# Kernel tuning notes

Measured on AMD Instinct MI355X. Metric: run time of the kernel, lower is better.

## Reference

```python
import jax, jax.numpy as jnp
import numpy as np

C = 64
K = 3  # kernel_size
B, H, W = 8, 128, 128


def conv2d(x, w, b, pad, groups=1):
    y = jax.lax.conv_general_dilated(
        x, w, window_strides=(1, 1), padding=[(pad, pad), (pad, pad)],
        feature_group_count=groups, dimension_numbers=('NCHW', 'OIHW', 'NCHW'))
    return y + b[None, :, None, None]


def setup_inputs() -> dict:
    key = jax.random.key(0)
    ks = jax.random.split(key, 11)
    s3 = 1.0 / np.sqrt(C * 9)  # kaiming-ish scale for 3x3 convs
    inp = {
        'x':  jax.random.normal(ks[0], (B, C, H, W), jnp.float32),
        'w0': jax.random.normal(ks[1], (C, C, 3, 3), jnp.float32) * s3,
        'b0': jax.random.normal(ks[2], (C,), jnp.float32) * 0.01,
        'w1': jax.random.normal(ks[3], (C, 1, 3, 3), jnp.float32) * (1.0 / 3.0),  # depthwise
        'b1': jax.random.normal(ks[4], (C,), jnp.float32) * 0.01,
        'w2': jax.random.normal(ks[5], (1, 1, K), jnp.float32) * (1.0 / np.sqrt(K)),  # conv1d over channel axis
        'b2': jax.random.normal(ks[6], (1,), jnp.float32) * 0.01,
        'w3': jax.random.normal(ks[7], (C * K * K, C, 1, 1), jnp.float32) * (1.0 / np.sqrt(C)),  # 1x1 -> dynamic filters
        'b3': jax.random.normal(ks[8], (C * K * K,), jnp.float32) * 0.01,
        'wf': jax.random.normal(ks[9], (C, C, 3, 3), jnp.float32) * s3,
        'bf': jax.random.normal(ks[10], (C,), jnp.float32) * 0.01,
    }
    return inp


def reference(x, w0, b0, w1, b1, w2, b2, w3, b3, wf, bf):
    b, c, h, w = x.shape
    pre = x
    # conv0: dense 3x3
    x0 = conv2d(x, w0, b0, pad=1)
    # conv1: depthwise 3x3
    x1 = conv2d(x0, w1, b1, pad=1, groups=c)
    # ECA-style channel attention: global avg pool -> conv1d over channel dim
    m = jnp.mean(x0, axis=(2, 3))  # [b, c]
    x2 = jax.lax.conv_general_dilated(
        m[:, None, :], w2, window_strides=(1,), padding=[(K // 2, K // 2)],
        dimension_numbers=('NCH', 'OIH', 'NCH')) + b2[None, :, None]  # [b, 1, c]
    out = x1 + x2[:, 0, :, None, None]  # broadcast [b,c,1,1] over h,w
    # conv3: 1x1 producing per-pixel dynamic filters [b, c*9, h, w]
    fil = jnp.einsum('oc,bchw->bohw', w3[:, :, 0, 0], out) + b3[None, :, None, None]
    filter_x = fil.reshape(b, c, K * K, h, w)
    # unfold(x0): 3x3 patches, channel-major then row-major kernel positions
    xp = jnp.pad(x0, ((0, 0), (0, 0), (1, 1), (1, 1)))
    unfold_x = jnp.stack(
        [xp[:, :, i:i + h, j:j + w] for i in range(3) for j in range(3)], axis=2)  # [b,c,9,h,w]
    out = jnp.sum(unfold_x * filter_x, axis=2)  # per-pixel dynamic conv
    out = jnp.where(out >= 0, out, 0.2 * out)  # LeakyReLU(0.2)
    out = conv2d(out, wf, bf, pad=1) + pre
    return out
```

## Files before the change

### kernel.cpp

```cpp
#include <hip/hip_runtime.h>

#define BB 8
#define C 64
#define HH 128
#define WW 128
#define HW (HH*WW)

#define TS 72
#define NPX 324

typedef __attribute__((ext_vector_type(8))) short short8;
typedef __attribute__((ext_vector_type(4))) short short4v;
typedef __attribute__((ext_vector_type(4))) float f32x4;

__device__ inline unsigned short f2bf(float f) {
    union { float f; unsigned u; } v; v.f = f;
    unsigned r = v.u + 0x7fff + ((v.u >> 16) & 1);
    return (unsigned short)(r >> 16);
}
__device__ inline float bf2f(unsigned short h) {
    union { unsigned u; float f; } v; v.u = ((unsigned)h) << 16;
    return v.f;
}

__global__ __launch_bounds__(256) void prep_kernel(
    const float* __restrict__ w0, const float* __restrict__ wf,
    const float* __restrict__ w3, const float* __restrict__ b3,
    unsigned short* __restrict__ wb0, unsigned short* __restrict__ wbf,
    unsigned short* __restrict__ wb3, float* __restrict__ b3r,
    float* __restrict__ m)
{
    const int t = blockIdx.x * 256 + threadIdx.x;
    for (int i = t; i < C*C*9; i += 32*256) {
        int p = i % 9; int rest = i / 9; int ci = rest % C; int oc = rest / C;
        wb0[(p*C + oc)*C + ci] = f2bf(w0[i]);
        wbf[(p*C + oc)*C + ci] = f2bf(wf[i]);
    }
    for (int i = t; i < 9*C*C; i += 32*256) {
        int j = i >> 12, oc = (i >> 6) & 63, k = i & 63;
        wb3[i] = f2bf(w3[(oc*9 + j)*C + k]);
    }
    for (int i = t; i < 9*C; i += 32*256) {
        int j = i >> 6, oc = i & 63;
        b3r[i] = b3[oc*9 + j];
    }
    for (int i = t; i < BB*C; i += 32*256) m[i] = 0.f;
}

__global__ __launch_bounds__(256) void conv0_kernel(
    const float* __restrict__ x,
    const unsigned short* __restrict__ wb,
    const float* __restrict__ bias,
    unsigned short* __restrict__ x0g)
{
    __shared__ unsigned short tile[NPX*TS];
    const int b  = blockIdx.z;
    const int h0 = blockIdx.y * 16;
    const int w0 = blockIdx.x * 16;
    const int t  = threadIdx.x;

    {
        const int pxi = t & 31, g = t >> 5;
        for (int px = pxi; px < NPX; px += 32) {
            int th = px / 18, tw = px - th*18;
            int gh = h0 + th - 1, gw = w0 + tw - 1;
            short8 v = {0,0,0,0,0,0,0,0};
            if ((unsigned)gh < HH && (unsigned)gw < WW) {
                const float* sp = x + ((size_t)(b*C + g*8)*HW + gh*WW + gw);
#pragma unroll
                for (int k = 0; k < 8; ++k) v[k] = (short)f2bf(sp[k*HW]);
            }
            *(short8*)&tile[px*TS + g*8] = v;
        }
    }
    __syncthreads();

    const int wid = t >> 6, ln = t & 63;
    const int l15 = ln & 15, q = ln >> 4;

    f32x4 acc[4][4];
#pragma unroll
    for (int nt = 0; nt < 4; ++nt)
#pragma unroll
        for (int mt = 0; mt < 4; ++mt) acc[nt][mt] = (f32x4){0.f,0.f,0.f,0.f};

#pragma unroll
    for (int p = 0; p < 9; ++p) {
        const int dh = p / 3, dw = p % 3;
#pragma unroll
        for (int ks = 0; ks < 2; ++ks) {
            short8 af[4];
#pragma unroll
            for (int mt = 0; mt < 4; ++mt)
                af[mt] = *(const short8*)&wb[((size_t)(p*C) + mt*16 + l15)*C + ks*32 + q*8];
            short8 bf[4];
#pragma unroll
            for (int nt = 0; nt < 4; ++nt)
                bf[nt] = *(const short8*)&tile[((wid*4+nt+dh)*18 + l15 + dw)*TS + ks*32 + q*8];
#pragma unroll
            for (int nt = 0; nt < 4; ++nt)
#pragma unroll
                for (int mt = 0; mt < 4; ++mt)
                    acc[nt][mt] = __builtin_amdgcn_mfma_f32_16x16x32_bf16(
                        af[mt], bf[nt], acc[nt][mt], 0, 0, 0);
        }
    }

#pragma unroll
    for (int nt = 0; nt < 4; ++nt) {
        const int hh = h0 + wid*4 + nt;
        const size_t base = ((size_t)(b*HW) + hh*WW + w0 + l15)*C;
#pragma unroll
        for (int mt = 0; mt < 4; ++mt) {
            const int oc0 = mt*16 + q*4;
            const float4 bv = *(const float4*)&bias[oc0];
            unsigned u0 = (unsigned)f2bf(acc[nt][mt][0] + bv.x)
                        | ((unsigned)f2bf(acc[nt][mt][1] + bv.y) << 16);
            unsigned u1 = (unsigned)f2bf(acc[nt][mt][2] + bv.z)
                        | ((unsigned)f2bf(acc[nt][mt][3] + bv.w) << 16);
            uint2 uu; uu.x = u0; uu.y = u1;
            *(uint2*)&x0g[base + oc0] = uu;
        }
    }
}

__global__ __launch_bounds__(256) void mean_kernel(
    const unsigned short* __restrict__ x0, float* __restrict__ m)
{
    const int b = blockIdx.x >> 4, slice = blockIdx.x & 15;
    const int t = threadIdx.x;
    const int pxi = t >> 3, g = t & 7;
    const unsigned short* base = x0 + ((size_t)b*HW + slice*1024)*C + g*8;
    float s[8];
#pragma unroll
    for (int k = 0; k < 8; ++k) s[k] = 0.f;
    for (int it = 0; it < 32; ++it) {
        short8 v = *(const short8*)&base[(size_t)(it*32 + pxi)*C];
#pragma unroll
        for (int k = 0; k < 8; ++k) s[k] += bf2f((unsigned short)v[k]);
    }
    __shared__ float red[32][64];
#pragma unroll
    for (int k = 0; k < 8; ++k) red[pxi][g*8+k] = s[k];
    __syncthreads();
    if (t < 64) {
        float acc = 0.f;
        for (int i = 0; i < 32; ++i) acc += red[i][t];
        atomicAdd(&m[b*C + t], acc * (1.f/(float)HW));
    }
}

__global__ __launch_bounds__(256, 4) void dw_eca_kernel(
    const unsigned short* __restrict__ x0,
    const float* __restrict__ w1, const float* __restrict__ b1,
    const float* __restrict__ w2, const float* __restrict__ b2,
    const float* __restrict__ m,
    unsigned short* __restrict__ aout)
{
    const int tg = blockIdx.x * 256 + threadIdx.x;
    const int b = tg >> 14, px = tg & 16383;
    const int h = px >> 7, w = px & 127;
    const unsigned short* xb = x0 + (size_t)(b*HW)*C;
    const float w2a = w2[0], w2b = w2[1], w2c = w2[2], b2v = b2[0];

#pragma unroll
    for (int g = 0; g < 8; ++g) {
        float dw8[8];
#pragma unroll
        for (int k = 0; k < 8; ++k) dw8[k] = 0.f;
#pragma unroll
        for (int j = 0; j < 9; ++j) {
            const int nh = h + j/3 - 1, nw = w + j%3 - 1;
            short8 v = {0,0,0,0,0,0,0,0};
            if ((unsigned)nh < HH && (unsigned)nw < WW)
                v = *(const short8*)&xb[(size_t)(nh*WW + nw)*C + g*8];
#pragma unroll
            for (int k = 0; k < 8; ++k)
                dw8[k] = fmaf(w1[(g*8+k)*9 + j], bf2f((unsigned short)v[k]), dw8[k]);
        }
        short8 o;
#pragma unroll
        for (int k = 0; k < 8; ++k) {
            const int c = g*8 + k;
            const float mc = m[b*C + c];
            const float mp = (c > 0)  ? m[b*C + c - 1] : 0.f;
            const float mn = (c < 63) ? m[b*C + c + 1] : 0.f;
            const float att = fmaf(w2a, mp, fmaf(w2b, mc, fmaf(w2c, mn, b2v)));
            o[k] = (short)f2bf(dw8[k] + b1[c] + att);
        }
        *(short8*)&aout[(size_t)(b*HW + px)*C + g*8] = o;
    }
}

__global__ __launch_bounds__(256) void dynconv_kernel(
    const unsigned short* __restrict__ x0,
    const unsigned short* __restrict__ aout,
    const unsigned short* __restrict__ wb3,
    const float* __restrict__ b3r,
    unsigned short* __restrict__ yg)
{
    __shared__ unsigned short tile[NPX*TS];
    const int b  = blockIdx.z;
    const int h0 = blockIdx.y * 16;
    const int w0 = blockIdx.x * 16;
    const int t  = threadIdx.x;

    {
        const int pxi = t & 31, g = t >> 5;
        for (int px = pxi; px < NPX; px += 32) {
            int th = px / 18, tw = px - th*18;
            int gh = h0 + th - 1, gw = w0 + tw - 1;
            short8 v = {0,0,0,0,0,0,0,0};
            if ((unsigned)gh < HH && (unsigned)gw < WW)
                v = *(const short8*)&x0[((size_t)(b*HW) + gh*WW + gw)*C + g*8];
            *(short8*)&tile[px*TS + g*8] = v;
        }
    }
    __syncthreads();

    const int wid = t >> 6, ln = t & 63;
    const int l15 = ln & 15, q = ln >> 4;
    const int rl0 = wid*4;

    short8 pfrag[4][2];
#pragma unroll
    for (int nt = 0; nt < 4; ++nt) {
        const size_t pbase = ((size_t)(b*HW) + (h0+rl0+nt)*WW + w0 + l15)*C;
#pragma unroll
        for (int ks = 0; ks < 2; ++ks)
            pfrag[nt][ks] = *(const short8*)&aout[pbase + ks*32 + q*8];
    }

#pragma unroll
    for (int og = 0; og < 4; ++og) {
        f32x4 yac[4];
#pragma unroll
        for (int nt = 0; nt < 4; ++nt) yac[nt] = (f32x4){0.f,0.f,0.f,0.f};

        for (int j = 0; j < 9; ++j) {
            const int dh = j / 3, dw = j - dh*3;
            const f32x4 seed = *(const f32x4*)&b3r[j*64 + og*16 + q*4];
            const size_t abase = ((size_t)(j*64 + og*16 + l15))*C;
            const short8 a0 = *(const short8*)&wb3[abase + q*8];
            const short8 a1 = *(const short8*)&wb3[abase + 32 + q*8];
#pragma unroll
            for (int nt = 0; nt < 4; ++nt) {
                f32x4 fil = __builtin_amdgcn_mfma_f32_16x16x32_bf16(
                    a0, pfrag[nt][0], seed, 0, 0, 0);
                fil = __builtin_amdgcn_mfma_f32_16x16x32_bf16(
                    a1, pfrag[nt][1], fil, 0, 0, 0);
                const short4v pv = *(const short4v*)
                    &tile[((rl0+nt+dh)*18 + l15 + dw)*TS + og*16 + q*4];
#pragma unroll
                for (int reg = 0; reg < 4; ++reg)
                    yac[nt][reg] = fmaf(fil[reg],
                        bf2f((unsigned short)pv[reg]), yac[nt][reg]);
            }
        }

#pragma unroll
        for (int nt = 0; nt < 4; ++nt) {
            const size_t base = ((size_t)(b*HW) + (h0+rl0+nt)*WW + w0 + l15)*C;
            f32x4 v = yac[nt];
#pragma unroll
            for (int reg = 0; reg < 4; ++reg)
                v[reg] = (v[reg] >= 0.f) ? v[reg] : 0.2f * v[reg];
            unsigned u0 = (unsigned)f2bf(v[0]) | ((unsigned)f2bf(v[1]) << 16);
            unsigned u1 = (unsigned)f2bf(v[2]) | ((unsigned)f2bf(v[3]) << 16);
            uint2 uu; uu.x = u0; uu.y = u1;
            *(uint2*)&yg[base + og*16 + q*4] = uu;
        }
    }
}

__global__ __launch_bounds__(256) void convf_kernel(
    const unsigned short* __restrict__ yg,
    const unsigned short* __restrict__ wb,
    const float* __restrict__ bias,
    const float* __restrict__ res,
    float* __restrict__ outg)
{
    __shared__ unsigned short tile[NPX*TS];
    const int b  = blockIdx.z;
    const int h0 = blockIdx.y * 16;
    const int w0 = blockIdx.x * 16;
    const int t  = threadIdx.x;

    {
        const int pxi = t & 31, g = t >> 5;
        for (int px = pxi; px < NPX; px += 32) {
            int th = px / 18, tw = px - th*18;
            int gh = h0 + th - 1, gw = w0 + tw - 1;
            short8 v = {0,0,0,0,0,0,0,0};
            if ((unsigned)gh < HH && (unsigned)gw < WW)
                v = *(const short8*)&yg[((size_t)(b*HW) + gh*WW + gw)*C + g*8];
            *(short8*)&tile[px*TS + g*8] = v;
        }
    }
    __syncthreads();

    const int wid = t >> 6, ln = t & 63;
    const int l15 = ln & 15, q = ln >> 4;

    f32x4 acc[4][4];
#pragma unroll
    for (int mg = 0; mg < 4; ++mg)
#pragma unroll
        for (int nt = 0; nt < 4; ++nt) acc[mg][nt] = (f32x4){0.f,0.f,0.f,0.f};

#pragma unroll
    for (int p = 0; p < 9; ++p) {
        const int dh = p / 3, dw = p % 3;
#pragma unroll
        for (int ks = 0; ks < 2; ++ks) {
            short8 bfrag[4];
#pragma unroll
            for (int nt = 0; nt < 4; ++nt)
                bfrag[nt] = *(const short8*)&wb[((size_t)(p*C) + nt*16 + l15)*C + ks*32 + q*8];
            short8 afrag[4];
#pragma unroll
            for (int mg = 0; mg < 4; ++mg)
                afrag[mg] = *(const short8*)&tile[((wid*4+mg+dh)*18 + l15 + dw)*TS + ks*32 + q*8];
#pragma unroll
            for (int mg = 0; mg < 4; ++mg)
#pragma unroll
                for (int nt = 0; nt < 4; ++nt)
                    acc[mg][nt] = __builtin_amdgcn_mfma_f32_16x16x32_bf16(
                        afrag[mg], bfrag[nt], acc[mg][nt], 0, 0, 0);
        }
    }

#pragma unroll
    for (int mg = 0; mg < 4; ++mg) {
        const int hh = h0 + wid*4 + mg;
#pragma unroll
        for (int nt = 0; nt < 4; ++nt) {
            const int oc = nt*16 + l15;
            const float bv = bias[oc];
            const size_t base = (size_t)(b*C + oc)*HW + hh*WW + w0 + q*4;
            const float4 rv = *(const float4*)&res[base];
            float4 ov;
            ov.x = acc[mg][nt][0] + bv + rv.x;
            ov.y = acc[mg][nt][1] + bv + rv.y;
            ov.z = acc[mg][nt][2] + bv + rv.z;
            ov.w = acc[mg][nt][3] + bv + rv.w;
            *(float4*)&outg[base] = ov;
        }
    }
}

extern "C" void kernel_launch(void* const* d_in, const int* in_sizes, int n_in,
                              void* d_out, int out_size, void* d_ws, size_t ws_size,
                              hipStream_t stream) {
    const float* x  = (const float*)d_in[0];
    const float* w0 = (const float*)d_in[1];
    const float* b0 = (const float*)d_in[2];
    const float* w1 = (const float*)d_in[3];
    const float* b1 = (const float*)d_in[4];
    const float* w2 = (const float*)d_in[5];
    const float* b2 = (const float*)d_in[6];
    const float* w3 = (const float*)d_in[7];
    const float* b3 = (const float*)d_in[8];
    const float* wf = (const float*)d_in[9];
    const float* bf = (const float*)d_in[10];
    float* out = (float*)d_out;

    unsigned short* x0  = (unsigned short*)d_ws;
    unsigned short* y   = x0  + (size_t)BB*HW*C;
    unsigned short* ao  = y   + (size_t)BB*HW*C;
    float*          m   = (float*)(ao + (size_t)BB*HW*C);
    unsigned short* wb0 = (unsigned short*)(m + BB*C);
    unsigned short* wbf = wb0 + 9*C*C;
    unsigned short* wb3 = wbf + 9*C*C;
    float*          b3r = (float*)(wb3 + 9*C*C);

    prep_kernel<<<32, 256, 0, stream>>>(w0, wf, w3, b3, wb0, wbf, wb3, b3r, m);
    conv0_kernel<<<dim3(8,8,8), 256, 0, stream>>>(x, wb0, b0, x0);
    mean_kernel<<<128, 256, 0, stream>>>(x0, m);
    dw_eca_kernel<<<512, 256, 0, stream>>>(x0, w1, b1, w2, b2, m, ao);
    dynconv_kernel<<<dim3(8,8,8), 256, 0, stream>>>(x0, ao, wb3, b3r, y);
    convf_kernel<<<dim3(8,8,8), 256, 0, stream>>>(y, wbf, bf, x, out);
}
```

Baseline: 252.7 us.

## Fuse depthwise+ECA into dynamic conv kernel and double block threads

The depthwise 3x3 conv plus ECA attention is now computed inside the dynamic-filter kernel from the already-loaded x0 halo tile. Its output is kept in a swizzled LDS buffer instead of a global intermediate, which removes one kernel launch and a full write and read of the activation tensor. conv0 and convf move to 512 threads per block, with each wave covering 2 rows instead of 4 and the output-channel groups split across waves in the fused kernel. The larger LDS footprint (about 80KB per block) and 512-thread blocks may lower occupancy.

```diff
diff --git a/kernel.cpp b/kernel.cpp
--- a/kernel.cpp
+++ b/kernel.cpp
@@ -47,7 +47,7 @@
     for (int i = t; i < BB*C; i += 32*256) m[i] = 0.f;
 }
 
-__global__ __launch_bounds__(256) void conv0_kernel(
+__global__ __launch_bounds__(512) void conv0_kernel(
     const float* __restrict__ x,
     const unsigned short* __restrict__ wb,
     const float* __restrict__ bias,
@@ -60,8 +60,8 @@
     const int t  = threadIdx.x;
 
     {
-        const int pxi = t & 31, g = t >> 5;
-        for (int px = pxi; px < NPX; px += 32) {
+        const int pxi = t & 63, g = t >> 6;
+        for (int px = pxi; px < NPX; px += 64) {
             int th = px / 18, tw = px - th*18;
             int gh = h0 + th - 1, gw = w0 + tw - 1;
             short8 v = {0,0,0,0,0,0,0,0};
@@ -78,9 +78,9 @@
     const int wid = t >> 6, ln = t & 63;
     const int l15 = ln & 15, q = ln >> 4;
 
-    f32x4 acc[4][4];
-#pragma unroll
-    for (int nt = 0; nt < 4; ++nt)
+    f32x4 acc[2][4];
+#pragma unroll
+    for (int nt = 0; nt < 2; ++nt)
 #pragma unroll
         for (int mt = 0; mt < 4; ++mt) acc[nt][mt] = (f32x4){0.f,0.f,0.f,0.f};
 
@@ -93,12 +93,12 @@
 #pragma unroll
             for (int mt = 0; mt < 4; ++mt)
                 af[mt] = *(const short8*)&wb[((size_t)(p*C) + mt*16 + l15)*C + ks*32 + q*8];
-            short8 bf[4];
-#pragma unroll
-            for (int nt = 0; nt < 4; ++nt)
-                bf[nt] = *(const short8*)&tile[((wid*4+nt+dh)*18 + l15 + dw)*TS + ks*32 + q*8];
-#pragma unroll
-            for (int nt = 0; nt < 4; ++nt)
+            short8 bf[2];
+#pragma unroll
+            for (int nt = 0; nt < 2; ++nt)
+                bf[nt] = *(const short8*)&tile[((wid*2+nt+dh)*18 + l15 + dw)*TS + ks*32 + q*8];
+#pragma unroll
+            for (int nt = 0; nt < 2; ++nt)
 #pragma unroll
                 for (int mt = 0; mt < 4; ++mt)
                     acc[nt][mt] = __builtin_amdgcn_mfma_f32_16x16x32_bf16(
@@ -107,8 +107,8 @@
     }
 
 #pragma unroll
-    for (int nt = 0; nt < 4; ++nt) {
-        const int hh = h0 + wid*4 + nt;
+    for (int nt = 0; nt < 2; ++nt) {
+        const int hh = h0 + wid*2 + nt;
         const size_t base = ((size_t)(b*HW) + hh*WW + w0 + l15)*C;
 #pragma unroll
         for (int mt = 0; mt < 4; ++mt) {
@@ -150,64 +150,25 @@
     }
 }
 
-__global__ __launch_bounds__(256, 4) void dw_eca_kernel(
+__global__ __launch_bounds__(512) void fused_dyn_kernel(
     const unsigned short* __restrict__ x0,
     const float* __restrict__ w1, const float* __restrict__ b1,
     const float* __restrict__ w2, const float* __restrict__ b2,
-    const float* __restrict__ m,
-    unsigned short* __restrict__ aout)
-{
-    const int tg = blockIdx.x * 256 + threadIdx.x;
-    const int b = tg >> 14, px = tg & 16383;
-    const int h = px >> 7, w = px & 127;
-    const unsigned short* xb = x0 + (size_t)(b*HW)*C;
-    const float w2a = w2[0], w2b = w2[1], w2c = w2[2], b2v = b2[0];
-
-#pragma unroll
-    for (int g = 0; g < 8; ++g) {
-        float dw8[8];
-#pragma unroll
-        for (int k = 0; k < 8; ++k) dw8[k] = 0.f;
-#pragma unroll
-        for (int j = 0; j < 9; ++j) {
-            const int nh = h + j/3 - 1, nw = w + j%3 - 1;
-            short8 v = {0,0,0,0,0,0,0,0};
-            if ((unsigned)nh < HH && (unsigned)nw < WW)
-                v = *(const short8*)&xb[(size_t)(nh*WW + nw)*C + g*8];
-#pragma unroll
-            for (int k = 0; k < 8; ++k)
-                dw8[k] = fmaf(w1[(g*8+k)*9 + j], bf2f((unsigned short)v[k]), dw8[k]);
-        }
-        short8 o;
-#pragma unroll
-        for (int k = 0; k < 8; ++k) {
-            const int c = g*8 + k;
-            const float mc = m[b*C + c];
-            const float mp = (c > 0)  ? m[b*C + c - 1] : 0.f;
-            const float mn = (c < 63) ? m[b*C + c + 1] : 0.f;
-            const float att = fmaf(w2a, mp, fmaf(w2b, mc, fmaf(w2c, mn, b2v)));
-            o[k] = (short)f2bf(dw8[k] + b1[c] + att);
-        }
-        *(short8*)&aout[(size_t)(b*HW + px)*C + g*8] = o;
-    }
-}
-
-__global__ __launch_bounds__(256) void dynconv_kernel(
-    const unsigned short* __restrict__ x0,
-    const unsigned short* __restrict__ aout,
     const unsigned short* __restrict__ wb3,
     const float* __restrict__ b3r,
+    const float* __restrict__ m,
     unsigned short* __restrict__ yg)
 {
     __shared__ unsigned short tile[NPX*TS];
+    __shared__ unsigned short alds[256*64];
     const int b  = blockIdx.z;
     const int h0 = blockIdx.y * 16;
     const int w0 = blockIdx.x * 16;
     const int t  = threadIdx.x;
 
     {
-        const int pxi = t & 31, g = t >> 5;
-        for (int px = pxi; px < NPX; px += 32) {
+        const int pxi = t & 63, g = t >> 6;
+        for (int px = pxi; px < NPX; px += 64) {
             int th = px / 18, tw = px - th*18;
             int gh = h0 + th - 1, gw = w0 + tw - 1;
             short8 v = {0,0,0,0,0,0,0,0};
@@ -218,21 +179,59 @@
     }
     __syncthreads();
 
+    {
+        const int px = t & 255, ghalf = t >> 8;
+        const int r = px >> 4, cc = px & 15;
+        const unsigned short* tb = tile + (r*18 + cc)*TS;
+        const float w2a = w2[0], w2b = w2[1], w2c = w2[2], b2v = b2[0];
+        const int sw = px & 7;
+#pragma unroll
+        for (int g = 0; g < 4; ++g) {
+            const int octet = ghalf*4 + g;
+            float dw8[8];
+#pragma unroll
+            for (int k = 0; k < 8; ++k) dw8[k] = 0.f;
+#pragma unroll
+            for (int j = 0; j < 9; ++j) {
+                short8 v = *(const short8*)&tb[((j/3)*18 + (j%3))*TS + octet*8];
+#pragma unroll
+                for (int k = 0; k < 8; ++k)
+                    dw8[k] = fmaf(w1[(octet*8+k)*9 + j],
+                                  bf2f((unsigned short)v[k]), dw8[k]);
+            }
+            short8 o;
+#pragma unroll
+            for (int k = 0; k < 8; ++k) {
+                const int c = octet*8 + k;
+                const float mc = m[b*C + c];
+                const float mp = (c > 0)  ? m[b*C + c - 1] : 0.f;
+                const float mn = (c < 63) ? m[b*C + c + 1] : 0.f;
+                const float att = fmaf(w2a, mp, fmaf(w2b, mc, fmaf(w2c, mn, b2v)));
+                o[k] = (short)f2bf(dw8[k] + b1[c] + att);
+            }
+            *(short8*)&alds[px*64 + ((octet ^ sw) * 8)] = o;
+        }
+    }
+    __syncthreads();
+
     const int wid = t >> 6, ln = t & 63;
     const int l15 = ln & 15, q = ln >> 4;
-    const int rl0 = wid*4;
+    const int rl0 = (wid & 3) * 4;
+    const int ogh = wid >> 2;
 
     short8 pfrag[4][2];
 #pragma unroll
     for (int nt = 0; nt < 4; ++nt) {
-        const size_t pbase = ((size_t)(b*HW) + (h0+rl0+nt)*WW + w0 + l15)*C;
+        const int p = (rl0 + nt)*16 + l15;
+        const int psw = p & 7;
 #pragma unroll
         for (int ks = 0; ks < 2; ++ks)
-            pfrag[nt][ks] = *(const short8*)&aout[pbase + ks*32 + q*8];
-    }
-
-#pragma unroll
-    for (int og = 0; og < 4; ++og) {
+            pfrag[nt][ks] = *(const short8*)&alds[p*64 + (((ks*4 + q) ^ psw) * 8)];
+    }
+
+#pragma unroll
+    for (int ogi = 0; ogi < 2; ++ogi) {
+        const int og = ogh*2 + ogi;
         f32x4 yac[4];
 #pragma unroll
         for (int nt = 0; nt < 4; ++nt) yac[nt] = (f32x4){0.f,0.f,0.f,0.f};
@@ -273,7 +272,7 @@
     }
 }
 
-__global__ __launch_bounds__(256) void convf_kernel(
+__global__ __launch_bounds__(512) void convf_kernel(
     const unsigned short* __restrict__ yg,
     const unsigned short* __restrict__ wb,
     const float* __restrict__ bias,
@@ -287,8 +286,8 @@
     const int t  = threadIdx.x;
 
     {
-        const int pxi = t & 31, g = t >> 5;
-        for (int px = pxi; px < NPX; px += 32) {
+        const int pxi = t & 63, g = t >> 6;
+        for (int px = pxi; px < NPX; px += 64) {
             int th = px / 18, tw = px - th*18;
             int gh = h0 + th - 1, gw = w0 + tw - 1;
             short8 v = {0,0,0,0,0,0,0,0};
@@ -302,9 +301,9 @@
     const int wid = t >> 6, ln = t & 63;
     const int l15 = ln & 15, q = ln >> 4;
 
-    f32x4 acc[4][4];
-#pragma unroll
-    for (int mg = 0; mg < 4; ++mg)
+    f32x4 acc[2][4];
+#pragma unroll
+    for (int mg = 0; mg < 2; ++mg)
 #pragma unroll
         for (int nt = 0; nt < 4; ++nt) acc[mg][nt] = (f32x4){0.f,0.f,0.f,0.f};
 
@@ -317,12 +316,12 @@
 #pragma unroll
             for (int nt = 0; nt < 4; ++nt)
                 bfrag[nt] = *(const short8*)&wb[((size_t)(p*C) + nt*16 + l15)*C + ks*32 + q*8];
-            short8 afrag[4];
-#pragma unroll
-            for (int mg = 0; mg < 4; ++mg)
-                afrag[mg] = *(const short8*)&tile[((wid*4+mg+dh)*18 + l15 + dw)*TS + ks*32 + q*8];
-#pragma unroll
-            for (int mg = 0; mg < 4; ++mg)
+            short8 afrag[2];
+#pragma unroll
+            for (int mg = 0; mg < 2; ++mg)
+                afrag[mg] = *(const short8*)&tile[((wid*2+mg+dh)*18 + l15 + dw)*TS + ks*32 + q*8];
+#pragma unroll
+            for (int mg = 0; mg < 2; ++mg)
 #pragma unroll
                 for (int nt = 0; nt < 4; ++nt)
                     acc[mg][nt] = __builtin_amdgcn_mfma_f32_16x16x32_bf16(
@@ -331,8 +330,8 @@
     }
 
 #pragma unroll
-    for (int mg = 0; mg < 4; ++mg) {
-        const int hh = h0 + wid*4 + mg;
+    for (int mg = 0; mg < 2; ++mg) {
+        const int hh = h0 + wid*2 + mg;
 #pragma unroll
         for (int nt = 0; nt < 4; ++nt) {
             const int oc = nt*16 + l15;
@@ -367,17 +366,16 @@
 
     unsigned short* x0  = (unsigned short*)d_ws;
     unsigned short* y   = x0  + (size_t)BB*HW*C;
-    unsigned short* ao  = y   + (size_t)BB*HW*C;
-    float*          m   = (float*)(ao + (size_t)BB*HW*C);
+    float*          m   = (float*)(y + (size_t)BB*HW*C);
     unsigned short* wb0 = (unsigned short*)(m + BB*C);
     unsigned short* wbf = wb0 + 9*C*C;
     unsigned short* wb3 = wbf + 9*C*C;
     float*          b3r = (float*)(wb3 + 9*C*C);
 
     prep_kernel<<<32, 256, 0, stream>>>(w0, wf, w3, b3, wb0, wbf, wb3, b3r, m);
-    conv0_kernel<<<dim3(8,8,8), 256, 0, stream>>>(x, wb0, b0, x0);
+    conv0_kernel<<<dim3(8,8,8), 512, 0, stream>>>(x, wb0, b0, x0);
     mean_kernel<<<128, 256, 0, stream>>>(x0, m);
-    dw_eca_kernel<<<512, 256, 0, stream>>>(x0, w1, b1, w2, b2, m, ao);
-    dynconv_kernel<<<dim3(8,8,8), 256, 0, stream>>>(x0, ao, wb3, b3r, y);
-    convf_kernel<<<dim3(8,8,8), 256, 0, stream>>>(y, wbf, bf, x, out);
-}
+    fused_dyn_kernel<<<dim3(8,8,8), 512, 0, stream>>>(
+        x0, w1, b1, w2, b2, wb3, b3r, m, y);
+    convf_kernel<<<dim3(8,8,8), 512, 0, stream>>>(y, wbf, bf, x, out);
+}
```

After: 246.5 us. 2.4% less time.
